# Kernel optimization log

Measured on AMD Instinct MI355X. Metric: run time of the kernel, lower is better.

Reference implementation:

```python
import jax, jax.numpy as jnp
import numpy as np

N, D, H = 8192, 64, 256

def setup_inputs() -> dict:
    key = jax.random.key(0)
    k0, k1, k2, k3, k4 = jax.random.split(key, 5)
    y = jax.random.normal(k0, (N, D), jnp.float32)
    t = jax.random.uniform(k1, (1,), jnp.float32)
    # diffeq MLP params (time-conditioned 1-hidden-layer tanh net)
    W1 = jax.random.normal(k2, (D, H), jnp.float32) / np.float32(np.sqrt(D))
    b1 = jnp.zeros((H,), jnp.float32)
    wt = jax.random.normal(k3, (H,), jnp.float32) * jnp.float32(0.1)
    W2 = jax.random.normal(k4, (H, D), jnp.float32) / np.float32(np.sqrt(H))
    b2 = jnp.zeros((D,), jnp.float32)
    return {"t": t, "y": y, "W1": W1, "b1": b1, "wt": wt, "W2": W2, "b2": b2}

def reference(t, y, W1, b1, wt, W2, b2):
    ts = t[0]

    def f_single(yi):  # yi: [D] -> dy_i: [D]
        h = jnp.tanh(yi @ W1 + ts * wt + b1)
        return h @ W2 + b2

    # dy = diffeq(t, y): batched forward pass
    h = jnp.tanh(y @ W1 + ts * wt + b1)          # [N, H]
    dy = h @ W2 + b2                              # [N, D]

    # brute-force divergence = trace of per-sample Jacobian d(dy_i)/d(y_i)
    # (replaces the O(D) looped torch.autograd.grad calls with one batched
    #  forward-mode Jacobian computation)
    div = jax.vmap(lambda yi: jnp.trace(jax.jacfwd(f_single)(yi)))(y)  # [N]

    # original returns (dy, -divergence.view(N,1)); concatenated for a single output
    return jnp.concatenate([dy, -div[:, None]], axis=1)  # [N, D+1]
```

## Files before the change

kernel.cpp:

```cpp
#include <hip/hip_runtime.h>

#define NROWS 8192
#define DDIM 64
#define HDIM 256
#define HPAD 264

using bf16x8 = __attribute__((ext_vector_type(8))) short;
using f32x4  = __attribute__((ext_vector_type(4))) float;

__device__ __forceinline__ unsigned short f2bf(float x) {
    unsigned u = __float_as_uint(x);
    u += 0x7FFFu + ((u >> 16) & 1u);
    return (unsigned short)(u >> 16);
}

__device__ __forceinline__ float fast_tanh(float x) {
    float e = __expf(2.0f * x);
    return 1.0f - 2.0f * __builtin_amdgcn_rcpf(e + 1.0f);
}

__global__ void prep_kernel(const float* __restrict__ t,
                            const float* __restrict__ W1,
                            const float* __restrict__ b1,
                            const float* __restrict__ wt,
                            const float* __restrict__ W2,
                            unsigned short* __restrict__ W1t,
                            unsigned short* __restrict__ W2t,
                            float* __restrict__ Cb,
                            float* __restrict__ Sv) {
    int gid = blockIdx.x * 256 + threadIdx.x;
    if (blockIdx.x < 64) {
        int m = gid >> 6, k = gid & 63;
        W1t[gid] = f2bf(W1[k * HDIM + m]);
    } else if (blockIdx.x < 128) {
        int i = gid - 16384;
        int n = i >> 8, k = i & 255;
        W2t[i] = f2bf(W2[k * DDIM + n]);
    } else {
        int m = threadIdx.x;
        Cb[m] = b1[m] + t[0] * wt[m];
        float s = 0.f;
        #pragma unroll
        for (int k = 0; k < DDIM; ++k) s += W1[k * HDIM + m] * W2[m * DDIM + k];
        Sv[m] = s;
    }
}

__global__ __launch_bounds__(256)
void ode_main(const float* __restrict__ y,
              const unsigned short* __restrict__ W1t,
              const unsigned short* __restrict__ W2t,
              const float* __restrict__ Cb,
              const float* __restrict__ Sv,
              const float* __restrict__ b2,
              float* __restrict__ out) {
    const int tid  = threadIdx.x;
    const int w    = tid >> 6;
    const int lane = tid & 63;
    const int l16  = lane & 15;
    const int quad = lane >> 4;
    const int row0 = blockIdx.x * 16;

    __shared__ __align__(16) unsigned short h_lds[16 * HPAD];
    __shared__ float dvp[64];

    bf16x8 afr[2];
    const float* yrow = y + (size_t)(row0 + l16) * DDIM;
    #pragma unroll
    for (int ks = 0; ks < 2; ++ks) {
        const float4 f0 = *(const float4*)(yrow + ks * 32 + quad * 8);
        const float4 f1 = *(const float4*)(yrow + ks * 32 + quad * 8 + 4);
        bf16x8 a;
        a[0] = (short)f2bf(f0.x); a[1] = (short)f2bf(f0.y);
        a[2] = (short)f2bf(f0.z); a[3] = (short)f2bf(f0.w);
        a[4] = (short)f2bf(f1.x); a[5] = (short)f2bf(f1.y);
        a[6] = (short)f2bf(f1.z); a[7] = (short)f2bf(f1.w);
        afr[ks] = a;
    }

    f32x4 acc[4];
    #pragma unroll
    for (int ct = 0; ct < 4; ++ct) acc[ct] = (f32x4){0.f, 0.f, 0.f, 0.f};

    #pragma unroll
    for (int ct = 0; ct < 4; ++ct) {
        const int m = w * 64 + ct * 16 + l16;
        #pragma unroll
        for (int ks = 0; ks < 2; ++ks) {
            bf16x8 b = *(const bf16x8*)(W1t + m * DDIM + ks * 32 + quad * 8);
            acc[ct] = __builtin_amdgcn_mfma_f32_16x16x32_bf16(afr[ks], b, acc[ct], 0, 0, 0);
        }
    }

    float dv[4] = {0.f, 0.f, 0.f, 0.f};
    #pragma unroll
    for (int ct = 0; ct < 4; ++ct) {
        const int m = w * 64 + ct * 16 + l16;
        const float cb = Cb[m];
        const float sv = Sv[m];
        #pragma unroll
        for (int r = 0; r < 4; ++r) {
            float z = acc[ct][r] + cb;
            float h = fast_tanh(z);
            dv[r] += (1.f - h * h) * sv;
            h_lds[(quad * 4 + r) * HPAD + m] = f2bf(h);
        }
    }
    #pragma unroll
    for (int off = 8; off; off >>= 1) {
        #pragma unroll
        for (int r = 0; r < 4; ++r) dv[r] += __shfl_down(dv[r], off, 16);
    }
    if (l16 == 0) {
        #pragma unroll
        for (int r = 0; r < 4; ++r) dvp[w * 16 + quad * 4 + r] = dv[r];
    }
    __syncthreads();

    f32x4 acc2 = (f32x4){0.f, 0.f, 0.f, 0.f};
    const int n = w * 16 + l16;
    #pragma unroll
    for (int ks = 0; ks < 8; ++ks) {
        bf16x8 a = *(const bf16x8*)(&h_lds[l16 * HPAD + ks * 32 + quad * 8]);
        bf16x8 b = *(const bf16x8*)(W2t + n * HDIM + ks * 32 + quad * 8);
        acc2 = __builtin_amdgcn_mfma_f32_16x16x32_bf16(a, b, acc2, 0, 0, 0);
    }
    const float b2v = b2[n];
    #pragma unroll
    for (int r = 0; r < 4; ++r) {
        const int row = quad * 4 + r;
        out[(size_t)(row0 + row) * (DDIM + 1) + n] = acc2[r] + b2v;
    }

    if (w == 0 && lane < 16) {
        float s = dvp[lane] + dvp[16 + lane] + dvp[32 + lane] + dvp[48 + lane];
        out[(size_t)(row0 + lane) * (DDIM + 1) + DDIM] = -s;
    }
}

extern "C" void kernel_launch(void* const* d_in, const int* in_sizes, int n_in,
                              void* d_out, int out_size, void* d_ws, size_t ws_size,
                              hipStream_t stream) {
    const float* t  = (const float*)d_in[0];
    const float* y  = (const float*)d_in[1];
    const float* W1 = (const float*)d_in[2];
    const float* b1 = (const float*)d_in[3];
    const float* wt = (const float*)d_in[4];
    const float* W2 = (const float*)d_in[5];
    const float* b2 = (const float*)d_in[6];
    float* out = (float*)d_out;

    unsigned short* W1t = (unsigned short*)d_ws;
    unsigned short* W2t = (unsigned short*)((char*)d_ws + 32768);
    float* Cb = (float*)((char*)d_ws + 65536);
    float* Sv = (float*)((char*)d_ws + 66560);

    prep_kernel<<<129, 256, 0, stream>>>(t, W1, b1, wt, W2, W1t, W2t, Cb, Sv);
    ode_main<<<NROWS / 16, 256, 0, stream>>>(y, W1t, W2t, Cb, Sv, b2, out);
}
```

Before: 74.91 us.

## Fuse weight prep into main kernel, converting fp32 weights to bf16 per block

Removes the separate prep kernel and its workspace round trip. Each of the 512 blocks now reads the fp32 W1/W2 directly with strided scalar loads, converts them to bf16 fragments in registers, and computes the trace vector and bias terms locally. This saves a kernel launch and the dependency between the two kernels. In exchange, the weight transpose and conversion work is repeated in every block, using uncoalesced gathers and extra registers.

```diff
diff --git a/kernel.cpp b/kernel.cpp
--- a/kernel.cpp
+++ b/kernel.cpp
@@ -19,41 +19,15 @@
     return 1.0f - 2.0f * __builtin_amdgcn_rcpf(e + 1.0f);
 }
 
-__global__ void prep_kernel(const float* __restrict__ t,
-                            const float* __restrict__ W1,
-                            const float* __restrict__ b1,
-                            const float* __restrict__ wt,
-                            const float* __restrict__ W2,
-                            unsigned short* __restrict__ W1t,
-                            unsigned short* __restrict__ W2t,
-                            float* __restrict__ Cb,
-                            float* __restrict__ Sv) {
-    int gid = blockIdx.x * 256 + threadIdx.x;
-    if (blockIdx.x < 64) {
-        int m = gid >> 6, k = gid & 63;
-        W1t[gid] = f2bf(W1[k * HDIM + m]);
-    } else if (blockIdx.x < 128) {
-        int i = gid - 16384;
-        int n = i >> 8, k = i & 255;
-        W2t[i] = f2bf(W2[k * DDIM + n]);
-    } else {
-        int m = threadIdx.x;
-        Cb[m] = b1[m] + t[0] * wt[m];
-        float s = 0.f;
-        #pragma unroll
-        for (int k = 0; k < DDIM; ++k) s += W1[k * HDIM + m] * W2[m * DDIM + k];
-        Sv[m] = s;
-    }
-}
-
 __global__ __launch_bounds__(256)
-void ode_main(const float* __restrict__ y,
-              const unsigned short* __restrict__ W1t,
-              const unsigned short* __restrict__ W2t,
-              const float* __restrict__ Cb,
-              const float* __restrict__ Sv,
-              const float* __restrict__ b2,
-              float* __restrict__ out) {
+void ode_fused(const float* __restrict__ t,
+               const float* __restrict__ y,
+               const float* __restrict__ W1,
+               const float* __restrict__ b1,
+               const float* __restrict__ wt,
+               const float* __restrict__ W2,
+               const float* __restrict__ b2,
+               float* __restrict__ out) {
     const int tid  = threadIdx.x;
     const int w    = tid >> 6;
     const int lane = tid & 63;
@@ -64,12 +38,59 @@
     __shared__ __align__(16) unsigned short h_lds[16 * HPAD];
     __shared__ float dvp[64];
 
-    bf16x8 afr[2];
     const float* yrow = y + (size_t)(row0 + l16) * DDIM;
+    float4 yf[4];
     #pragma unroll
     for (int ks = 0; ks < 2; ++ks) {
-        const float4 f0 = *(const float4*)(yrow + ks * 32 + quad * 8);
-        const float4 f1 = *(const float4*)(yrow + ks * 32 + quad * 8 + 4);
+        yf[2 * ks]     = *(const float4*)(yrow + ks * 32 + quad * 8);
+        yf[2 * ks + 1] = *(const float4*)(yrow + ks * 32 + quad * 8 + 4);
+    }
+
+    const float t0   = t[0];
+    const int  mbase = w * 64;
+    const int  n     = w * 16 + l16;
+
+    bf16x8 bfr2[8];
+    #pragma unroll
+    for (int ks = 0; ks < 8; ++ks) {
+        const int k0 = ks * 32 + quad * 8;
+        bf16x8 b;
+        #pragma unroll
+        for (int j = 0; j < 8; ++j) b[j] = (short)f2bf(W2[(k0 + j) * DDIM + n]);
+        bfr2[ks] = b;
+    }
+
+    bf16x8 bfr1[4][2];
+    float  cb[4], sv[4];
+    #pragma unroll
+    for (int ct = 0; ct < 4; ++ct) {
+        const int m = mbase + ct * 16 + l16;
+        float s = 0.f;
+        #pragma unroll
+        for (int ks = 0; ks < 2; ++ks) {
+            const int k0 = ks * 32 + quad * 8;
+            const float4 r0 = *(const float4*)(W2 + m * DDIM + k0);
+            const float4 r1 = *(const float4*)(W2 + m * DDIM + k0 + 4);
+            const float w2r[8] = {r0.x, r0.y, r0.z, r0.w, r1.x, r1.y, r1.z, r1.w};
+            bf16x8 b;
+            #pragma unroll
+            for (int j = 0; j < 8; ++j) {
+                const float w1v = W1[(k0 + j) * HDIM + m];
+                b[j] = (short)f2bf(w1v);
+                s += w1v * w2r[j];
+            }
+            bfr1[ct][ks] = b;
+        }
+        s += __shfl_xor(s, 16);
+        s += __shfl_xor(s, 32);
+        sv[ct] = s;
+        cb[ct] = b1[m] + t0 * wt[m];
+    }
+
+    bf16x8 afr[2];
+    #pragma unroll
+    for (int ks = 0; ks < 2; ++ks) {
+        const float4 f0 = yf[2 * ks], f1 = yf[2 * ks + 1];
         bf16x8 a;
         a[0] = (short)f2bf(f0.x); a[1] = (short)f2bf(f0.y);
         a[2] = (short)f2bf(f0.z); a[3] = (short)f2bf(f0.w);
@@ -84,25 +105,20 @@
 
     #pragma unroll
     for (int ct = 0; ct < 4; ++ct) {
-        const int m = w * 64 + ct * 16 + l16;
         #pragma unroll
-        for (int ks = 0; ks < 2; ++ks) {
-            bf16x8 b = *(const bf16x8*)(W1t + m * DDIM + ks * 32 + quad * 8);
-            acc[ct] = __builtin_amdgcn_mfma_f32_16x16x32_bf16(afr[ks], b, acc[ct], 0, 0, 0);
-        }
+        for (int ks = 0; ks < 2; ++ks)
+            acc[ct] = __builtin_amdgcn_mfma_f32_16x16x32_bf16(afr[ks], bfr1[ct][ks], acc[ct], 0, 0, 0);
     }
 
     float dv[4] = {0.f, 0.f, 0.f, 0.f};
     #pragma unroll
     for (int ct = 0; ct < 4; ++ct) {
-        const int m = w * 64 + ct * 16 + l16;
-        const float cb = Cb[m];
-        const float sv = Sv[m];
+        const int m = mbase + ct * 16 + l16;
         #pragma unroll
         for (int r = 0; r < 4; ++r) {
-            float z = acc[ct][r] + cb;
+            float z = acc[ct][r] + cb[ct];
             float h = fast_tanh(z);
-            dv[r] += (1.f - h * h) * sv;
+            dv[r] += (1.f - h * h) * sv[ct];
             h_lds[(quad * 4 + r) * HPAD + m] = f2bf(h);
         }
     }
@@ -118,12 +134,10 @@
     __syncthreads();
 
     f32x4 acc2 = (f32x4){0.f, 0.f, 0.f, 0.f};
-    const int n = w * 16 + l16;
     #pragma unroll
     for (int ks = 0; ks < 8; ++ks) {
         bf16x8 a = *(const bf16x8*)(&h_lds[l16 * HPAD + ks * 32 + quad * 8]);
-        bf16x8 b = *(const bf16x8*)(W2t + n * HDIM + ks * 32 + quad * 8);
-        acc2 = __builtin_amdgcn_mfma_f32_16x16x32_bf16(a, b, acc2, 0, 0, 0);
+        acc2 = __builtin_amdgcn_mfma_f32_16x16x32_bf16(a, bfr2[ks], acc2, 0, 0, 0);
     }
     const float b2v = b2[n];
     #pragma unroll
@@ -150,11 +164,7 @@
     const float* b2 = (const float*)d_in[6];
     float* out = (float*)d_out;
 
-    unsigned short* W1t = (unsigned short*)d_ws;
-    unsigned short* W2t = (unsigned short*)((char*)d_ws + 32768);
-    float* Cb = (float*)((char*)d_ws + 65536);
-    float* Sv = (float*)((char*)d_ws + 66560);
+    (void)d_ws; (void)ws_size;
 
-    prep_kernel<<<129, 256, 0, stream>>>(t, W1, b1, wt, W2, W1t, W2t, Cb, Sv);
-    ode_main<<<NROWS / 16, 256, 0, stream>>>(y, W1t, W2t, Cb, Sv, b2, out);
+    ode_fused<<<NROWS / 16, 256, 0, stream>>>(t, y, W1, b1, wt, W2, b2, out);
 }
```

Result: no change. 73.46 us (-1.9%).
